# Optimization experiments

Hardware: AMD Instinct MI355X
Metric: run time of the kernel (lower is better)

## Reference

```python
import jax, jax.numpy as jnp
import numpy as np

DROPOUT_RATE = 0.1  # reference runs deterministically (dropout disabled), matching eval-mode math


def setup_inputs() -> dict:
    key = jax.random.key(0)
    k1, k2, k3 = jax.random.split(key, 3)
    BH, S, D = 32, 2048, 64   # batch*heads, seq_len, d_head
    B = 2                      # true batch (mask batch dim)
    q = jax.random.normal(k1, (BH, S, D), dtype=jnp.float32)
    k = jax.random.normal(k2, (BH, S, D), dtype=jnp.float32)
    v = jax.random.normal(k3, (BH, S, D), dtype=jnp.float32)
    mask = jnp.zeros((B, S, S), dtype=jnp.float32)  # additive mask
    return {"q": q, "k": k, "v": v, "mask": mask}


def reference(q, k, v, mask):
    # Scaled dot-product attention with additive mask.
    # q,k,v: [BH, S, D]; mask: [B, S, S], tiled along batch to BH.
    dk = jnp.asarray(k.shape[-1], dtype=jnp.float32)
    scores = jnp.einsum('bqd,bkd->bqk', q, k) / jnp.sqrt(dk)  # [BH, S, S]
    reps = q.shape[0] // mask.shape[0]
    mask_t = jnp.tile(mask, (reps, 1, 1))                     # [BH, S, S]
    attn = jax.nn.softmax(scores + mask_t, axis=-1)
    out = jnp.einsum('bqk,bkd->bqd', attn, v)                 # [BH, S, D]
    # K.dropout omitted: deterministic reference (eval mode / identity)
    return out
```

## Files before the change

kernel.cpp:

```cpp
#include <hip/hip_runtime.h>


constexpr int cBH = 32;
constexpr int cS  = 2048;
constexpr int cD  = 64;
constexpr int cQT = 128;
constexpr int cNP = cS / 128;

typedef __bf16 bf16x8 __attribute__((ext_vector_type(8)));
typedef __bf16 bf16x4 __attribute__((ext_vector_type(4)));
typedef float  f32x4  __attribute__((ext_vector_type(4)));

__device__ __forceinline__ unsigned short bfbits(float f) {
    return __builtin_bit_cast(unsigned short, (__bf16)f);
}
__device__ __forceinline__ bf16x4 pack4(f32x4 a) {
    bf16x4 r;
    r[0] = (__bf16)a[0]; r[1] = (__bf16)a[1];
    r[2] = (__bf16)a[2]; r[3] = (__bf16)a[3];
    return r;
}
__device__ __forceinline__ bf16x8 pack8s(f32x4 a, f32x4 b, float s) {
    bf16x8 r;
    r[0] = (__bf16)(a[0]*s); r[1] = (__bf16)(a[1]*s);
    r[2] = (__bf16)(a[2]*s); r[3] = (__bf16)(a[3]*s);
    r[4] = (__bf16)(b[0]*s); r[5] = (__bf16)(b[1]*s);
    r[6] = (__bf16)(b[2]*s); r[7] = (__bf16)(b[3]*s);
    return r;
}
__device__ __forceinline__ int fkey(int row) {
    return ((row & 7) ^ ((row >> 3) << 1)) & 7;
}
__device__ __forceinline__ int gkey(int d) {
    return (d ^ (d >> 3)) & 7;
}

__global__ __launch_bounds__(256, 2)
void sdpa_flash_kernel(const float* __restrict__ q,
                       const float* __restrict__ k,
                       const float* __restrict__ v,
                       const float* __restrict__ mask,
                       float* __restrict__ out)
{
    __shared__ unsigned short sK[2][64 * 64];
    __shared__ unsigned short sV[2][64 * 64];
    __shared__ unsigned short sP[4][2][32 * 64];

    const int tid  = threadIdx.x;
    const int wv   = tid >> 6;
    const int lane = tid & 63;
    const int quad = lane >> 4;
    const int ln   = lane & 15;

    const int fid = blockIdx.x;
    const int bh  = (fid & 7) | ((fid >> 7) << 3);
    const int qb  = ((fid >> 3) & 15) * cQT;
    const int mb  = bh & 1;

    const float L2E = 1.4426950408889634f;

    bf16x8 aq[2][2];
#pragma unroll
    for (int mg = 0; mg < 2; ++mg) {
        const float* qp = q + ((size_t)bh * cS + qb + wv * 32 + mg * 16 + ln) * cD + quad * 8;
        aq[mg][0] = pack8s(*(const f32x4*)(qp),      *(const f32x4*)(qp + 4),  0.125f * L2E);
        aq[mg][1] = pack8s(*(const f32x4*)(qp + 32), *(const f32x4*)(qp + 36), 0.125f * L2E);
    }

    f32x4 acc[2][4];
    float lsum[2][4];
#pragma unroll
    for (int mg = 0; mg < 2; ++mg)
#pragma unroll
        for (int t = 0; t < 4; ++t) {
            acc[mg][t] = (f32x4){0.f, 0.f, 0.f, 0.f};
            lsum[mg][t] = 0.f;
        }

    const int sr0 = tid >> 4;
    const int c4  = (tid & 15) << 2;
    const int ka0 = sr0 * 64 + (((c4 >> 3) ^ (sr0 & 7)) << 3) + (c4 & 7);
    const float* kg = k + (size_t)bh * cS * cD;
    const float* vg = v + (size_t)bh * cS * cD;
    const float* mq = mask + (size_t)mb * cS * cS
                           + (size_t)(qb + wv * 32 + quad * 4) * cS + ln;

#pragma unroll
    for (int t = 0; t < 2; ++t)
#pragma unroll
        for (int j = 0; j < 4; ++j) {
            f32x4 kj = *(const f32x4*)(kg + t * 4096 + j * 1024 + tid * 4);
            f32x4 vj = *(const f32x4*)(vg + t * 4096 + j * 1024 + tid * 4);
            *(bf16x4*)&sK[t][ka0 + j * 1024] = pack4(kj);
#pragma unroll
            for (int i = 0; i < 4; ++i) {
                int d = c4 + i;
                sV[t][d * 64 + ((((j * 2) + (sr0 >> 3)) ^ gkey(d)) << 3) + (sr0 & 7)]
                    = bfbits(vj[i]);
            }
        }

    for (int pt = 0; pt < cNP; ++pt) {
        const int base = pt * 2;
        const bool more = (pt + 1 < cNP);
        const int nb = more ? base + 2 : base;

        f32x4 KPe[4], VPe[4], KPo[4], VPo[4];
#pragma unroll
        for (int j = 0; j < 4; ++j) {
            KPe[j] = *(const f32x4*)(kg + (size_t)nb * 4096 + j * 1024 + tid * 4);
            VPe[j] = *(const f32x4*)(vg + (size_t)nb * 4096 + j * 1024 + tid * 4);
            KPo[j] = *(const f32x4*)(kg + (size_t)(nb + 1) * 4096 + j * 1024 + tid * 4);
            VPo[j] = *(const f32x4*)(vg + (size_t)(nb + 1) * 4096 + j * 1024 + tid * 4);
        }
        float mcE[2][4][4], mcO[2][4][4];
#pragma unroll
        for (int mg = 0; mg < 2; ++mg)
#pragma unroll
            for (int nt = 0; nt < 4; ++nt)
#pragma unroll
                for (int r = 0; r < 4; ++r) {
                    const float* mrow = mq + (size_t)(mg * 16 + r) * cS + base * 64 + nt * 16;
                    mcE[mg][nt][r] = mrow[0];
                    mcO[mg][nt][r] = mrow[64];
                }

        __syncthreads();

        float pE[2][4][4], pO[2][4][4];
#pragma unroll
        for (int nt = 0; nt < 4; ++nt) {
            const int rb = (nt * 16 + ln) * 64;
            const int x0 = (quad ^ (ln & 7)) << 3;
            const int x1 = ((4 | quad) ^ (ln & 7)) << 3;
            bf16x8 be0 = *(const bf16x8*)(&sK[0][rb + x0]);
            bf16x8 be1 = *(const bf16x8*)(&sK[0][rb + x1]);
            bf16x8 bo0 = *(const bf16x8*)(&sK[1][rb + x0]);
            bf16x8 bo1 = *(const bf16x8*)(&sK[1][rb + x1]);
            f32x4 ce0 = (f32x4){0.f,0.f,0.f,0.f}, ce1 = ce0, co0 = ce0, co1 = ce0;
            ce0 = __builtin_amdgcn_mfma_f32_16x16x32_bf16(aq[0][0], be0, ce0, 0, 0, 0);
            ce1 = __builtin_amdgcn_mfma_f32_16x16x32_bf16(aq[1][0], be0, ce1, 0, 0, 0);
            co0 = __builtin_amdgcn_mfma_f32_16x16x32_bf16(aq[0][0], bo0, co0, 0, 0, 0);
            co1 = __builtin_amdgcn_mfma_f32_16x16x32_bf16(aq[1][0], bo0, co1, 0, 0, 0);
            ce0 = __builtin_amdgcn_mfma_f32_16x16x32_bf16(aq[0][1], be1, ce0, 0, 0, 0);
            ce1 = __builtin_amdgcn_mfma_f32_16x16x32_bf16(aq[1][1], be1, ce1, 0, 0, 0);
            co0 = __builtin_amdgcn_mfma_f32_16x16x32_bf16(aq[0][1], bo1, co0, 0, 0, 0);
            co1 = __builtin_amdgcn_mfma_f32_16x16x32_bf16(aq[1][1], bo1, co1, 0, 0, 0);
#pragma unroll
            for (int r = 0; r < 4; ++r) {
                pE[0][nt][r] = __builtin_amdgcn_exp2f(fmaf(mcE[0][nt][r], L2E, ce0[r]));
                pE[1][nt][r] = __builtin_amdgcn_exp2f(fmaf(mcE[1][nt][r], L2E, ce1[r]));
                pO[0][nt][r] = __builtin_amdgcn_exp2f(fmaf(mcO[0][nt][r], L2E, co0[r]));
                pO[1][nt][r] = __builtin_amdgcn_exp2f(fmaf(mcO[1][nt][r], L2E, co1[r]));
            }
        }
#pragma unroll
        for (int mg = 0; mg < 2; ++mg)
#pragma unroll
            for (int r = 0; r < 4; ++r)
                lsum[mg][r] += (pE[mg][0][r] + pE[mg][1][r]) + (pE[mg][2][r] + pE[mg][3][r])
                             + (pO[mg][0][r] + pO[mg][1][r]) + (pO[mg][2][r] + pO[mg][3][r]);

#pragma unroll
        for (int mg = 0; mg < 2; ++mg)
#pragma unroll
            for (int nt = 0; nt < 4; ++nt)
#pragma unroll
                for (int r = 0; r < 4; ++r) {
                    int row = mg * 16 + quad * 4 + r;
                    int blk = ((nt * 2 + (ln >> 3)) ^ fkey(row)) << 3;
                    sP[wv][0][row * 64 + blk + (ln & 7)] = bfbits(pE[mg][nt][r]);
                    sP[wv][1][row * 64 + blk + (ln & 7)] = bfbits(pO[mg][nt][r]);
                }

#pragma unroll
        for (int t = 0; t < 2; ++t) {
            const unsigned short* sPt = &sP[wv][t][0];
            const unsigned short* sVt = sV[t];
#pragma unroll
            for (int ks = 0; ks < 2; ++ks) {
                bf16x8 ap0 = *(const bf16x8*)(
                    &sPt[ln * 64 + ((((ks << 2) | quad) ^ fkey(ln)) << 3)]);
                bf16x8 ap1 = *(const bf16x8*)(
                    &sPt[(16 + ln) * 64 + ((((ks << 2) | quad) ^ fkey(16 + ln)) << 3)]);
#pragma unroll
                for (int dt = 0; dt < 4; ++dt) {
                    int d = dt * 16 + ln;
                    bf16x8 bv = *(const bf16x8*)(
                        &sVt[d * 64 + ((((ks << 2) | quad) ^ gkey(d)) << 3)]);
                    acc[0][dt] = __builtin_amdgcn_mfma_f32_16x16x32_bf16(ap0, bv, acc[0][dt], 0, 0, 0);
                    acc[1][dt] = __builtin_amdgcn_mfma_f32_16x16x32_bf16(ap1, bv, acc[1][dt], 0, 0, 0);
                }
            }
        }

        __syncthreads();

        if (more) {
#pragma unroll
            for (int j = 0; j < 4; ++j) {
                *(bf16x4*)&sK[0][ka0 + j * 1024] = pack4(KPe[j]);
                *(bf16x4*)&sK[1][ka0 + j * 1024] = pack4(KPo[j]);
#pragma unroll
                for (int i = 0; i < 4; ++i) {
                    int d = c4 + i;
                    int va = d * 64 + ((((j * 2) + (sr0 >> 3)) ^ gkey(d)) << 3) + (sr0 & 7);
                    sV[0][va] = bfbits(VPe[j][i]);
                    sV[1][va] = bfbits(VPo[j][i]);
                }
            }
        }
    }

#pragma unroll
    for (int off = 1; off < 16; off <<= 1)
#pragma unroll
        for (int mg = 0; mg < 2; ++mg)
#pragma unroll
            for (int r = 0; r < 4; ++r)
                lsum[mg][r] += __shfl_xor(lsum[mg][r], off, 64);
#pragma unroll
    for (int mg = 0; mg < 2; ++mg) {
        float rl[4];
#pragma unroll
        for (int r = 0; r < 4; ++r) rl[r] = 1.0f / lsum[mg][r];
#pragma unroll
        for (int dt = 0; dt < 4; ++dt)
#pragma unroll
            for (int r = 0; r < 4; ++r)
                out[((size_t)bh * cS + qb + wv * 32 + mg * 16 + quad * 4 + r) * cD
                    + dt * 16 + ln] = acc[mg][dt][r] * rl[r];
    }
}

extern "C" void kernel_launch(void* const* d_in, const int* in_sizes, int n_in,
                              void* d_out, int out_size, void* d_ws, size_t ws_size,
                              hipStream_t stream) {
    const float* q = (const float*)d_in[0];
    const float* k = (const float*)d_in[1];
    const float* v = (const float*)d_in[2];
    const float* m = (const float*)d_in[3];
    float* o = (float*)d_out;
    sdpa_flash_kernel<<<dim3(512), 256, 0, stream>>>(q, k, v, m, o);
}
```

Measured before the change: 172.9 us.

## Keep softmax probabilities in registers using 32x32 MFMA and permlane swaps

Switches both matmuls from 16x16x32 to 32x32x16 bf16 MFMA. QK^T is computed transposed, with K as the A operand, so each lane holds probabilities in the layout the PV MFMA needs once v_permlane32_swap shuffles them. This removes the per-wave sP shared-memory store and reload and its swizzling. In exchange, the mask is now loaded inside the compute loop as 16-byte vectors per row rather than prefetched before the barrier, which may expose global-load latency and changes coalescing.

```diff
diff --git a/kernel.cpp b/kernel.cpp
--- a/kernel.cpp
+++ b/kernel.cpp
@@ -10,6 +10,8 @@
 typedef __bf16 bf16x8 __attribute__((ext_vector_type(8)));
 typedef __bf16 bf16x4 __attribute__((ext_vector_type(4)));
 typedef float  f32x4  __attribute__((ext_vector_type(4)));
+typedef float  f32x16 __attribute__((ext_vector_type(16)));
+typedef unsigned int u32x4 __attribute__((ext_vector_type(4)));
 
 __device__ __forceinline__ unsigned short bfbits(float f) {
     return __builtin_bit_cast(unsigned short, (__bf16)f);
@@ -27,9 +29,6 @@
     r[4] = (__bf16)(b[0]*s); r[5] = (__bf16)(b[1]*s);
     r[6] = (__bf16)(b[2]*s); r[7] = (__bf16)(b[3]*s);
     return r;
-}
-__device__ __forceinline__ int fkey(int row) {
-    return ((row & 7) ^ ((row >> 3) << 1)) & 7;
 }
 __device__ __forceinline__ int gkey(int d) {
     return (d ^ (d >> 3)) & 7;
@@ -44,13 +43,13 @@
 {
     __shared__ unsigned short sK[2][64 * 64];
     __shared__ unsigned short sV[2][64 * 64];
-    __shared__ unsigned short sP[4][2][32 * 64];
 
     const int tid  = threadIdx.x;
     const int wv   = tid >> 6;
     const int lane = tid & 63;
-    const int quad = lane >> 4;
-    const int ln   = lane & 15;
+    const int l31  = lane & 31;
+    const int h    = lane >> 5;
+    const int swk  = (lane & 7) ^ (((lane >> 3) & 1) << 2);
 
     const int fid = blockIdx.x;
     const int bh  = (fid & 7) | ((fid >> 7) << 3);
@@ -59,31 +58,32 @@
 
     const float L2E = 1.4426950408889634f;
 
-    bf16x8 aq[2][2];
-#pragma unroll
-    for (int mg = 0; mg < 2; ++mg) {
-        const float* qp = q + ((size_t)bh * cS + qb + wv * 32 + mg * 16 + ln) * cD + quad * 8;
-        aq[mg][0] = pack8s(*(const f32x4*)(qp),      *(const f32x4*)(qp + 4),  0.125f * L2E);
-        aq[mg][1] = pack8s(*(const f32x4*)(qp + 32), *(const f32x4*)(qp + 36), 0.125f * L2E);
+    bf16x8 aq[4];
+    {
+        const float* qp = q + ((size_t)bh * cS + qb + wv * 32 + l31) * cD + h * 8;
+#pragma unroll
+        for (int dc = 0; dc < 4; ++dc)
+            aq[dc] = pack8s(*(const f32x4*)(qp + dc * 16),
+                            *(const f32x4*)(qp + dc * 16 + 4), 0.125f * L2E);
     }
 
-    f32x4 acc[2][4];
-    float lsum[2][4];
-#pragma unroll
-    for (int mg = 0; mg < 2; ++mg)
-#pragma unroll
-        for (int t = 0; t < 4; ++t) {
-            acc[mg][t] = (f32x4){0.f, 0.f, 0.f, 0.f};
-            lsum[mg][t] = 0.f;
-        }
+    f32x16 acc[2] = {};
+    float lsum = 0.f;
 
     const int sr0 = tid >> 4;
     const int c4  = (tid & 15) << 2;
-    const int ka0 = sr0 * 64 + (((c4 >> 3) ^ (sr0 & 7)) << 3) + (c4 & 7);
+    const int ka0 = sr0 * 64
+        + ((((c4 >> 3) ^ (sr0 & 7) ^ (((sr0 >> 3) & 1) << 2)) << 3))
+        + (c4 & 7);
     const float* kg = k + (size_t)bh * cS * cD;
     const float* vg = v + (size_t)bh * cS * cD;
     const float* mq = mask + (size_t)mb * cS * cS
-                           + (size_t)(qb + wv * 32 + quad * 4) * cS + ln;
+                           + (size_t)(qb + wv * 32 + l31) * cS + h * 4;
+
+    const int g0 = gkey(l31);
+    const int g1 = gkey(32 + l31);
+    const int vb0 = l31 * 64;
+    const int vb1 = (32 + l31) * 64;
 
 #pragma unroll
     for (int t = 0; t < 2; ++t)
@@ -113,83 +113,62 @@
             KPo[j] = *(const f32x4*)(kg + (size_t)(nb + 1) * 4096 + j * 1024 + tid * 4);
             VPo[j] = *(const f32x4*)(vg + (size_t)(nb + 1) * 4096 + j * 1024 + tid * 4);
         }
-        float mcE[2][4][4], mcO[2][4][4];
-#pragma unroll
-        for (int mg = 0; mg < 2; ++mg)
-#pragma unroll
-            for (int nt = 0; nt < 4; ++nt)
-#pragma unroll
-                for (int r = 0; r < 4; ++r) {
-                    const float* mrow = mq + (size_t)(mg * 16 + r) * cS + base * 64 + nt * 16;
-                    mcE[mg][nt][r] = mrow[0];
-                    mcO[mg][nt][r] = mrow[64];
-                }
 
         __syncthreads();
 
-        float pE[2][4][4], pO[2][4][4];
-#pragma unroll
-        for (int nt = 0; nt < 4; ++nt) {
-            const int rb = (nt * 16 + ln) * 64;
-            const int x0 = (quad ^ (ln & 7)) << 3;
-            const int x1 = ((4 | quad) ^ (ln & 7)) << 3;
-            bf16x8 be0 = *(const bf16x8*)(&sK[0][rb + x0]);
-            bf16x8 be1 = *(const bf16x8*)(&sK[0][rb + x1]);
-            bf16x8 bo0 = *(const bf16x8*)(&sK[1][rb + x0]);
-            bf16x8 bo1 = *(const bf16x8*)(&sK[1][rb + x1]);
-            f32x4 ce0 = (f32x4){0.f,0.f,0.f,0.f}, ce1 = ce0, co0 = ce0, co1 = ce0;
-            ce0 = __builtin_amdgcn_mfma_f32_16x16x32_bf16(aq[0][0], be0, ce0, 0, 0, 0);
-            ce1 = __builtin_amdgcn_mfma_f32_16x16x32_bf16(aq[1][0], be0, ce1, 0, 0, 0);
-            co0 = __builtin_amdgcn_mfma_f32_16x16x32_bf16(aq[0][0], bo0, co0, 0, 0, 0);
-            co1 = __builtin_amdgcn_mfma_f32_16x16x32_bf16(aq[1][0], bo0, co1, 0, 0, 0);
-            ce0 = __builtin_amdgcn_mfma_f32_16x16x32_bf16(aq[0][1], be1, ce0, 0, 0, 0);
-            ce1 = __builtin_amdgcn_mfma_f32_16x16x32_bf16(aq[1][1], be1, ce1, 0, 0, 0);
-            co0 = __builtin_amdgcn_mfma_f32_16x16x32_bf16(aq[0][1], bo1, co0, 0, 0, 0);
-            co1 = __builtin_amdgcn_mfma_f32_16x16x32_bf16(aq[1][1], bo1, co1, 0, 0, 0);
-#pragma unroll
-            for (int r = 0; r < 4; ++r) {
-                pE[0][nt][r] = __builtin_amdgcn_exp2f(fmaf(mcE[0][nt][r], L2E, ce0[r]));
-                pE[1][nt][r] = __builtin_amdgcn_exp2f(fmaf(mcE[1][nt][r], L2E, ce1[r]));
-                pO[0][nt][r] = __builtin_amdgcn_exp2f(fmaf(mcO[0][nt][r], L2E, co0[r]));
-                pO[1][nt][r] = __builtin_amdgcn_exp2f(fmaf(mcO[1][nt][r], L2E, co1[r]));
-            }
-        }
-#pragma unroll
-        for (int mg = 0; mg < 2; ++mg)
-#pragma unroll
-            for (int r = 0; r < 4; ++r)
-                lsum[mg][r] += (pE[mg][0][r] + pE[mg][1][r]) + (pE[mg][2][r] + pE[mg][3][r])
-                             + (pO[mg][0][r] + pO[mg][1][r]) + (pO[mg][2][r] + pO[mg][3][r]);
-
-#pragma unroll
-        for (int mg = 0; mg < 2; ++mg)
-#pragma unroll
-            for (int nt = 0; nt < 4; ++nt)
-#pragma unroll
-                for (int r = 0; r < 4; ++r) {
-                    int row = mg * 16 + quad * 4 + r;
-                    int blk = ((nt * 2 + (ln >> 3)) ^ fkey(row)) << 3;
-                    sP[wv][0][row * 64 + blk + (ln & 7)] = bfbits(pE[mg][nt][r]);
-                    sP[wv][1][row * 64 + blk + (ln & 7)] = bfbits(pO[mg][nt][r]);
-                }
-
 #pragma unroll
         for (int t = 0; t < 2; ++t) {
-            const unsigned short* sPt = &sP[wv][t][0];
+            const unsigned short* sKt = sK[t];
             const unsigned short* sVt = sV[t];
 #pragma unroll
-            for (int ks = 0; ks < 2; ++ks) {
-                bf16x8 ap0 = *(const bf16x8*)(
-                    &sPt[ln * 64 + ((((ks << 2) | quad) ^ fkey(ln)) << 3)]);
-                bf16x8 ap1 = *(const bf16x8*)(
-                    &sPt[(16 + ln) * 64 + ((((ks << 2) | quad) ^ fkey(16 + ln)) << 3)]);
-#pragma unroll
-                for (int dt = 0; dt < 4; ++dt) {
-                    int d = dt * 16 + ln;
-                    bf16x8 bv = *(const bf16x8*)(
-                        &sVt[d * 64 + ((((ks << 2) | quad) ^ gkey(d)) << 3)]);
-                    acc[0][dt] = __builtin_amdgcn_mfma_f32_16x16x32_bf16(ap0, bv, acc[0][dt], 0, 0, 0);
-                    acc[1][dt] = __builtin_amdgcn_mfma_f32_16x16x32_bf16(ap1, bv, acc[1][dt], 0, 0, 0);
+            for (int gg = 0; gg < 2; ++gg) {
+                const float* mrow = mq + (size_t)(base + t) * 64 + gg * 32;
+                f32x4 mk[4];
+#pragma unroll
+                for (int j = 0; j < 4; ++j)
+                    mk[j] = *(const f32x4*)(mrow + j * 8);
+
+                const int rb = (gg * 32 + l31) * 64;
+                bf16x8 kf[4];
+#pragma unroll
+                for (int dc = 0; dc < 4; ++dc)
+                    kf[dc] = *(const bf16x8*)(&sKt[rb + (((dc * 2 + h) ^ swk) << 3)]);
+                f32x16 s = {};
+#pragma unroll
+                for (int dc = 0; dc < 4; ++dc)
+                    s = __builtin_amdgcn_mfma_f32_32x32x16_bf16(kf[dc], aq[dc], s, 0, 0, 0);
+
+                float p[16];
+#pragma unroll
+                for (int r = 0; r < 16; ++r)
+                    p[r] = __builtin_amdgcn_exp2f(fmaf(mk[r >> 2][r & 3], L2E, s[r]));
+#pragma unroll
+                for (int r = 0; r < 16; ++r)
+                    lsum += p[r];
+
+                unsigned int pk[8];
+#pragma unroll
+                for (int i = 0; i < 8; ++i)
+                    pk[i] = (unsigned int)bfbits(p[2 * i])
+                          | ((unsigned int)bfbits(p[2 * i + 1]) << 16);
+                asm("v_permlane32_swap_b32 %0, %1" : "+v"(pk[0]), "+v"(pk[2]));
+                asm("v_permlane32_swap_b32 %0, %1" : "+v"(pk[1]), "+v"(pk[3]));
+                asm("v_permlane32_swap_b32 %0, %1" : "+v"(pk[4]), "+v"(pk[6]));
+                asm("v_permlane32_swap_b32 %0, %1" : "+v"(pk[5]), "+v"(pk[7]));
+                u32x4 ua = {pk[0], pk[1], pk[2], pk[3]};
+                u32x4 ub = {pk[4], pk[5], pk[6], pk[7]};
+                bf16x8 fA0 = __builtin_bit_cast(bf16x8, ua);
+                bf16x8 fA1 = __builtin_bit_cast(bf16x8, ub);
+
+#pragma unroll
+                for (int kc = 0; kc < 2; ++kc) {
+                    const int kb = gg * 4 + kc * 2 + h;
+                    bf16x8 bv0 = *(const bf16x8*)(&sVt[vb0 + ((kb ^ g0) << 3)]);
+                    bf16x8 bv1 = *(const bf16x8*)(&sVt[vb1 + ((kb ^ g1) << 3)]);
+                    acc[0] = __builtin_amdgcn_mfma_f32_32x32x16_bf16(
+                        kc ? fA1 : fA0, bv0, acc[0], 0, 0, 0);
+                    acc[1] = __builtin_amdgcn_mfma_f32_32x32x16_bf16(
+                        kc ? fA1 : fA0, bv1, acc[1], 0, 0, 0);
                 }
             }
         }
@@ -212,24 +191,14 @@
         }
     }
 
-#pragma unroll
-    for (int off = 1; off < 16; off <<= 1)
-#pragma unroll
-        for (int mg = 0; mg < 2; ++mg)
-#pragma unroll
-            for (int r = 0; r < 4; ++r)
-                lsum[mg][r] += __shfl_xor(lsum[mg][r], off, 64);
-#pragma unroll
-    for (int mg = 0; mg < 2; ++mg) {
-        float rl[4];
-#pragma unroll
-        for (int r = 0; r < 4; ++r) rl[r] = 1.0f / lsum[mg][r];
-#pragma unroll
-        for (int dt = 0; dt < 4; ++dt)
-#pragma unroll
-            for (int r = 0; r < 4; ++r)
-                out[((size_t)bh * cS + qb + wv * 32 + mg * 16 + quad * 4 + r) * cD
-                    + dt * 16 + ln] = acc[mg][dt][r] * rl[r];
+    lsum += __shfl_xor(lsum, 32, 64);
+#pragma unroll
+    for (int r = 0; r < 16; ++r) {
+        const int qrow = (r & 3) + 8 * (r >> 2) + 4 * h;
+        const float rl = 1.0f / __shfl(lsum, qrow, 64);
+        float* op = out + ((size_t)bh * cS + qb + wv * 32 + qrow) * cD + l31;
+        op[0]  = acc[0][r] * rl;
+        op[32] = acc[1][r] * rl;
     }
 }
 
```

New measurement: 182.5 us. +5.5%, slower.
